# Optimization experiments

Measured on AMD Instinct MI355X. Metric: run time of the kernel, lower is better.

The kernel has to match this reference:

```python
import jax, jax.numpy as jnp
import numpy as np

D_MODEL = 1280
NUM_HEADS = 16
GROUPS = 5
D_K = D_MODEL // NUM_HEADS  # 80
B, S = 4, 1024


def setup_inputs() -> dict:
    key = jax.random.key(0)
    ks = jax.random.split(key, 12)
    lim_dk = 1.0 / np.sqrt(D_K)
    lim_dm = 1.0 / np.sqrt(D_MODEL)
    return {
        "src": jax.random.normal(ks[0], (B, S, D_MODEL), jnp.float32),
        "k": jax.random.normal(ks[1], (B, S, D_MODEL), jnp.float32),
        "v": jax.random.normal(ks[2], (B, S, D_MODEL), jnp.float32),
        # per-head Linear(d_k, d_k) stacked: weight [H, d_k(out), d_k(in)], bias [H, d_k]
        "Wq": jax.random.uniform(ks[3], (NUM_HEADS, D_K, D_K), jnp.float32, -lim_dk, lim_dk),
        "bq": jax.random.uniform(ks[4], (NUM_HEADS, D_K), jnp.float32, -lim_dk, lim_dk),
        "Wk": jax.random.uniform(ks[5], (NUM_HEADS, D_K, D_K), jnp.float32, -lim_dk, lim_dk),
        "bk": jax.random.uniform(ks[6], (NUM_HEADS, D_K), jnp.float32, -lim_dk, lim_dk),
        "Wv": jax.random.uniform(ks[7], (NUM_HEADS, D_K, D_K), jnp.float32, -lim_dk, lim_dk),
        "bv": jax.random.uniform(ks[8], (NUM_HEADS, D_K), jnp.float32, -lim_dk, lim_dk),
        # output Linear(d_model, d_model)
        "Wo": jax.random.uniform(ks[9], (D_MODEL, D_MODEL), jnp.float32, -lim_dm, lim_dm),
        "bo": jax.random.uniform(ks[10], (D_MODEL,), jnp.float32, -lim_dm, lim_dm),
    }


def reference(src, k, v, Wq, bq, Wk, bk, Wv, bv, Wo, bo):
    # NOTE: original module ignores k, v args; q/k/v all derived from src.
    b, s, d = src.shape
    cpg = d // GROUPS
    # channel shuffle: [B,S,G,C] -> [B,S,C,G] -> [B,S,D]
    x = src.reshape(b, s, GROUPS, cpg).swapaxes(-1, -2).reshape(b, s, d)
    # split heads: [B, H, S, d_k]
    xh = x.reshape(b, s, NUM_HEADS, D_K).transpose(0, 2, 1, 3)
    # per-head distinct linears, batched over heads (torch Linear: x @ W.T + b)
    q = jnp.einsum("bhsd,hed->bhse", xh, Wq) + bq[None, :, None, :]
    kk = jnp.einsum("bhsd,hed->bhse", xh, Wk) + bk[None, :, None, :]
    vv = jnp.einsum("bhsd,hed->bhse", xh, Wv) + bv[None, :, None, :]
    scores = jnp.einsum("bhqd,bhkd->bhqk", q, kk) / jnp.sqrt(jnp.float32(D_K))
    p = jax.nn.softmax(scores, axis=-1)
    heads = jnp.einsum("bhqk,bhkd->bhqd", p, vv)
    concat = heads.transpose(0, 2, 1, 3).reshape(b, s, d)
    return concat @ Wo.T + bo
```

## Files before the change

kernel.cpp:

```cpp
#include <hip/hip_runtime.h>
#include <hip/hip_bf16.h>

#define D_MODEL 1280
#define NUM_HEADS 16
#define D_K 80
#define DP 96
#define SEQ 1024
#define BATCH 4
#define BH (BATCH*NUM_HEADS)

typedef __hip_bfloat16 bf16;
typedef short short8 __attribute__((ext_vector_type(8)));
typedef short short4v __attribute__((ext_vector_type(4)));
typedef float f32x4 __attribute__((ext_vector_type(4)));

__device__ __forceinline__ float b2f(bf16 x) { return __bfloat162float(x); }
__device__ __forceinline__ bf16 f2b(float x) { return __float2bfloat16(x); }
__device__ __forceinline__ short bbits(float x) {
    union { bf16 b; short s; } u; u.b = __float2bfloat16(x); return u.s;
}

#define MFMA16(a, b, c) __builtin_amdgcn_mfma_f32_16x16x32_bf16(a, b, c, 0, 0, 0)

__global__ __launch_bounds__(256) void cvtw_kernel(
    const float* __restrict__ Wq, const float* __restrict__ Wk,
    const float* __restrict__ Wv, bf16* __restrict__ Wcat)
{
    int idx = blockIdx.x * 256 + threadIdx.x;
    int col = idx % 96;
    int row = (idx / 96) % 240;
    int h   = idx / (96 * 240);
    int mat = row / 80, e = row % 80;
    const float* W = (mat == 0) ? Wq : (mat == 1) ? Wk : Wv;
    float v = (col < 80) ? W[(size_t)(h * 80 + e) * 80 + col] : 0.f;
    Wcat[idx] = f2b(v);
}

__global__ __launch_bounds__(256) void cvt_kernel(
    const float* __restrict__ Wo, bf16* __restrict__ Wb)
{
    int idx = (blockIdx.x * 256 + threadIdx.x) * 4;
    float4 v = *(const float4*)(Wo + idx);
    Wb[idx]     = f2b(v.x);
    Wb[idx + 1] = f2b(v.y);
    Wb[idx + 2] = f2b(v.z);
    Wb[idx + 3] = f2b(v.w);
}

__global__ __launch_bounds__(256) void qkv_kernel(
    const float* __restrict__ src,
    const float* __restrict__ bq, const float* __restrict__ bk,
    const float* __restrict__ bv, const bf16* __restrict__ Wcat,
    bf16* __restrict__ Qb, bf16* __restrict__ Kb, bf16* __restrict__ Vg)
{
    __shared__ bf16 Xs[128 * 104];
    const int h = blockIdx.y;
    const int b = blockIdx.x >> 3;
    const int s0 = (blockIdx.x & 7) * 128;
    const int tid = threadIdx.x;
    const int wave = tid >> 6, lane = tid & 63;
    const int lquad = lane >> 4, lcol = lane & 15;
    const int bh = b * NUM_HEADS + h;

    #pragma unroll
    for (int it = 0; it < 10; it++) {
        int idx = tid + it * 256;
        int i = idx / 20, rem = idx % 20, c = rem >> 2, q4 = rem & 3;
        float4 v = *(const float4*)(src + (size_t)(b * SEQ + s0 + i) * D_MODEL
                                    + c * 256 + h * 16 + q4 * 4);
        bf16* x = Xs + i * 104 + c;
        x[(q4 * 4 + 0) * 5] = f2b(v.x);
        x[(q4 * 4 + 1) * 5] = f2b(v.y);
        x[(q4 * 4 + 2) * 5] = f2b(v.z);
        x[(q4 * 4 + 3) * 5] = f2b(v.w);
    }
    {
        int i = tid >> 1, half = tid & 1;
        *(uint4*)(Xs + i * 104 + 80 + half * 8) = make_uint4(0, 0, 0, 0);
    }
    __syncthreads();

    short8 xf[2][3];
    #pragma unroll
    for (int mt = 0; mt < 2; mt++)
        #pragma unroll
        for (int ks = 0; ks < 3; ks++)
            xf[mt][ks] = *(const short8*)(Xs + (wave*32 + mt*16 + lcol)*104 + ks*32 + lquad*8);

    const bf16* Wh = Wcat + (size_t)h * 240 * 96;
    const float qscale = 1.4426950408889634f * 0.11180339887498949f;

    #pragma unroll
    for (int mat = 0; mat < 2; mat++) {
        const bf16* Wm = Wh + mat * 80 * 96;
        short8 wf[5][3];
        #pragma unroll
        for (int n = 0; n < 5; n++)
            #pragma unroll
            for (int ks = 0; ks < 3; ks++)
                wf[n][ks] = *(const short8*)(Wm + (n*16 + lcol)*96 + ks*32 + lquad*8);

        f32x4 acc[2][5];
        #pragma unroll
        for (int mt = 0; mt < 2; mt++)
            #pragma unroll
            for (int n = 0; n < 5; n++)
                #pragma unroll
                for (int r = 0; r < 4; r++) acc[mt][n][r] = 0.f;

        #pragma unroll
        for (int ks = 0; ks < 3; ks++)
            #pragma unroll
            for (int n = 0; n < 5; n++) {
                acc[0][n] = MFMA16(xf[0][ks], wf[n][ks], acc[0][n]);
                acc[1][n] = MFMA16(xf[1][ks], wf[n][ks], acc[1][n]);
            }

        const float* bias = (mat == 0) ? bq : bk;
        bf16* Out = (mat == 0) ? Qb : Kb;
        const float scale = (mat == 0) ? qscale : 1.f;
        #pragma unroll
        for (int n = 0; n < 5; n++) {
            float bb = bias[h * 80 + n * 16 + lcol];
            #pragma unroll
            for (int mt = 0; mt < 2; mt++)
                #pragma unroll
                for (int r = 0; r < 4; r++) {
                    int srow = s0 + wave*32 + mt*16 + lquad*4 + r;
                    Out[((size_t)bh * SEQ + srow) * DP + n*16 + lcol] =
                        f2b((acc[mt][n][r] + bb) * scale);
                }
        }
    }
    {
        int i = tid >> 1, half = tid & 1;
        size_t row = ((size_t)bh * SEQ + s0 + i) * DP + 80 + half * 8;
        *(uint4*)(Qb + row) = make_uint4(0, 0, 0, 0);
        *(uint4*)(Kb + row) = make_uint4(0, 0, 0, 0);
    }

    {
        const bf16* Wm = Wh + 2 * 80 * 96;
        short8 wf[5][3];
        #pragma unroll
        for (int m = 0; m < 5; m++)
            #pragma unroll
            for (int ks = 0; ks < 3; ks++)
                wf[m][ks] = *(const short8*)(Wm + (m*16 + lcol)*96 + ks*32 + lquad*8);

        f32x4 acc[5][2];
        #pragma unroll
        for (int m = 0; m < 5; m++)
            #pragma unroll
            for (int nt = 0; nt < 2; nt++)
                #pragma unroll
                for (int r = 0; r < 4; r++) acc[m][nt][r] = 0.f;

        #pragma unroll
        for (int ks = 0; ks < 3; ks++)
            #pragma unroll
            for (int m = 0; m < 5; m++) {
                acc[m][0] = MFMA16(wf[m][ks], xf[0][ks], acc[m][0]);
                acc[m][1] = MFMA16(wf[m][ks], xf[1][ks], acc[m][1]);
            }

        #pragma unroll
        for (int m = 0; m < 5; m++) {
            float4 bb4 = *(const float4*)(bv + h * 80 + m * 16 + lquad * 4);
            float bb[4] = {bb4.x, bb4.y, bb4.z, bb4.w};
            #pragma unroll
            for (int nt = 0; nt < 2; nt++)
                #pragma unroll
                for (int r = 0; r < 4; r++) {
                    int e = m*16 + lquad*4 + r;
                    int token = s0 + wave*32 + nt*16 + lcol;
                    Vg[((size_t)bh * D_K + e) * SEQ + token] =
                        f2b(acc[m][nt][r] + bb[r]);
                }
        }
    }
}

__global__ __launch_bounds__(128) void attn_kernel(
    const bf16* __restrict__ Qb, const bf16* __restrict__ Kb,
    const bf16* __restrict__ Vg, bf16* __restrict__ Cc)
{
    __shared__ char smem[38144];
    bf16* Qs = (bf16*)smem;
    bf16* Ks = (bf16*)(smem + 13312);
    bf16* Vt = (bf16*)(smem + 26624);

    const int tid = threadIdx.x;
    const int wave = tid >> 6, lane = tid & 63;
    const int lquad = lane >> 4, lcol = lane & 15;
    const int bh = blockIdx.x;
    const int b = bh >> 4, h = bh & 15;
    const int q0 = blockIdx.y * 64;

    {
        const uint4* qg = (const uint4*)(Qb + ((size_t)bh * SEQ + q0) * DP);
        #pragma unroll
        for (int i = 0; i < 6; i++) {
            int idx = tid + i * 128, r = idx / 12, c = idx % 12;
            *(uint4*)(Qs + r * 104 + c * 8) = qg[idx];
        }
    }
    __syncthreads();

    short8 qf[2][3];
    #pragma unroll
    for (int nt = 0; nt < 2; nt++)
        #pragma unroll
        for (int ks = 0; ks < 3; ks++)
            qf[nt][ks] = *(const short8*)(Qs + (wave*32 + nt*16 + lcol)*104 + ks*32 + lquad*8);

    f32x4 Oacc[2][5];
    #pragma unroll
    for (int mt = 0; mt < 2; mt++)
        #pragma unroll
        for (int ne = 0; ne < 5; ne++)
            #pragma unroll
            for (int r = 0; r < 4; r++) Oacc[mt][ne][r] = 0.f;

    float lsum[2] = {0.f, 0.f};
    bf16* Pw = (bf16*)(smem + wave * 4608);

    for (int kt = 0; kt < 16; kt++) {
        __syncthreads();
        {
            const uint4* kg = (const uint4*)(Kb + ((size_t)bh * SEQ + kt * 64) * DP);
            #pragma unroll
            for (int i = 0; i < 6; i++) {
                int idx = tid + i * 128, r = idx / 12, c = idx % 12;
                *(uint4*)(Ks + r * 104 + c * 8) = kg[idx];
            }
        }
        #pragma unroll
        for (int i = 0; i < 5; i++) {
            int idx = tid + i * 128;
            int e = idx >> 3, c = idx & 7;
            *(uint4*)(Vt + e * 72 + c * 8) =
                *(const uint4*)(Vg + ((size_t)bh * D_K + e) * SEQ + kt * 64 + c * 8);
        }
        __syncthreads();

        f32x4 st[4][2];
        #pragma unroll
        for (int mt = 0; mt < 4; mt++)
            #pragma unroll
            for (int nt = 0; nt < 2; nt++)
                #pragma unroll
                for (int r = 0; r < 4; r++) st[mt][nt][r] = 0.f;

        #pragma unroll
        for (int ks = 0; ks < 3; ks++) {
            #pragma unroll
            for (int mt = 0; mt < 4; mt++) {
                short8 af = *(const short8*)(Ks + (mt*16 + lcol)*104 + ks*32 + lquad*8);
                st[mt][0] = MFMA16(af, qf[0][ks], st[mt][0]);
                st[mt][1] = MFMA16(af, qf[1][ks], st[mt][1]);
            }
        }

        #pragma unroll
        for (int nt = 0; nt < 2; nt++) {
            #pragma unroll
            for (int mt = 0; mt < 4; mt++) {
                short4v pk;
                #pragma unroll
                for (int r = 0; r < 4; r++) {
                    float p = __builtin_amdgcn_exp2f(st[mt][nt][r]);
                    lsum[nt] += p;
                    pk[r] = bbits(p);
                }
                *(short4v*)(Pw + (nt*16 + lcol)*72 + mt*16 + lquad*4) = pk;
            }
        }

        #pragma unroll
        for (int js = 0; js < 2; js++) {
            short8 pf[2];
            #pragma unroll
            for (int mt = 0; mt < 2; mt++)
                pf[mt] = *(const short8*)(Pw + (mt*16 + lcol)*72 + js*32 + lquad*8);
            #pragma unroll
            for (int ne = 0; ne < 5; ne++) {
                short8 vf = *(const short8*)(Vt + (ne*16 + lcol)*72 + js*32 + lquad*8);
                Oacc[0][ne] = MFMA16(pf[0], vf, Oacc[0][ne]);
                Oacc[1][ne] = MFMA16(pf[1], vf, Oacc[1][ne]);
            }
        }
    }

    float inv[2];
    #pragma unroll
    for (int nt = 0; nt < 2; nt++) {
        float s = lsum[nt];
        s += __shfl_xor(s, 16);
        s += __shfl_xor(s, 32);
        inv[nt] = 1.f / s;
    }
    #pragma unroll
    for (int mt = 0; mt < 2; mt++) {
        f32x4 li;
        #pragma unroll
        for (int r = 0; r < 4; r++)
            li[r] = __shfl(inv[mt], (lane & 48) | (lquad*4 + r));
        #pragma unroll
        for (int ne = 0; ne < 5; ne++)
            #pragma unroll
            for (int r = 0; r < 4; r++) {
                int s_row = q0 + wave*32 + mt*16 + lquad*4 + r;
                int e = ne*16 + lcol;
                Cc[(size_t)(b * SEQ + s_row) * D_MODEL + h * D_K + e] =
                    f2b(Oacc[mt][ne][r] * li[r]);
            }
    }
}

__global__ __launch_bounds__(256) void proj_kernel(
    const bf16* __restrict__ Cc, const bf16* __restrict__ Wb,
    const float* __restrict__ bo, float* __restrict__ out)
{
    __shared__ bf16 As[128 * 72];
    __shared__ bf16 Bs[128 * 72];
    const int tid = threadIdx.x;
    const int wave = tid >> 6, lane = tid & 63;
    const int lquad = lane >> 4, lcol = lane & 15;
    const int t0 = blockIdx.x * 128, o0 = blockIdx.y * 128;
    const int mrow = (wave & 1) * 64, ncol = (wave >> 1) * 64;

    f32x4 acc[4][4];
    #pragma unroll
    for (int mt = 0; mt < 4; mt++)
        #pragma unroll
        for (int nt = 0; nt < 4; nt++)
            #pragma unroll
            for (int r = 0; r < 4; r++) acc[mt][nt][r] = 0.f;

    for (int kc = 0; kc < 20; kc++) {
        __syncthreads();
        #pragma unroll
        for (int i = 0; i < 4; i++) {
            int idx = tid + i * 256;
            int r = idx >> 3, c = idx & 7;
            *(uint4*)(As + r * 72 + c * 8) =
                *(const uint4*)(Cc + (size_t)(t0 + r) * D_MODEL + kc * 64 + c * 8);
            *(uint4*)(Bs + r * 72 + c * 8) =
                *(const uint4*)(Wb + (size_t)(o0 + r) * D_MODEL + kc * 64 + c * 8);
        }
        __syncthreads();
        #pragma unroll
        for (int ks = 0; ks < 2; ks++) {
            short8 am[4], bn[4];
            #pragma unroll
            for (int t = 0; t < 4; t++) {
                am[t] = *(const short8*)(As + (mrow + t*16 + lcol)*72 + ks*32 + lquad*8);
                bn[t] = *(const short8*)(Bs + (ncol + t*16 + lcol)*72 + ks*32 + lquad*8);
            }
            #pragma unroll
            for (int mt = 0; mt < 4; mt++)
                #pragma unroll
                for (int nt = 0; nt < 4; nt++)
                    acc[mt][nt] = MFMA16(am[mt], bn[nt], acc[mt][nt]);
        }
    }

    #pragma unroll
    for (int nt = 0; nt < 4; nt++) {
        float bias = bo[o0 + ncol + nt*16 + lcol];
        #pragma unroll
        for (int mt = 0; mt < 4; mt++)
            #pragma unroll
            for (int r = 0; r < 4; r++)
                out[(size_t)(t0 + mrow + mt*16 + lquad*4 + r) * D_MODEL
                    + o0 + ncol + nt*16 + lcol] = acc[mt][nt][r] + bias;
    }
}

extern "C" void kernel_launch(void* const* d_in, const int* in_sizes, int n_in,
                              void* d_out, int out_size, void* d_ws, size_t ws_size,
                              hipStream_t stream) {
    const float* src = (const float*)d_in[0];
    const float* Wq = (const float*)d_in[3];
    const float* bq = (const float*)d_in[4];
    const float* Wk = (const float*)d_in[5];
    const float* bk = (const float*)d_in[6];
    const float* Wv = (const float*)d_in[7];
    const float* bv = (const float*)d_in[8];
    const float* Wo = (const float*)d_in[9];
    const float* bo = (const float*)d_in[10];
    float* out = (float*)d_out;

    char* ws = (char*)d_ws;
    bf16* Qb = (bf16*)(ws);
    bf16* Kb = (bf16*)(ws + (size_t)12582912);
    bf16* Vg = (bf16*)(ws + (size_t)25165824);
    bf16* Cc = (bf16*)(ws + (size_t)35651584);
    bf16* Wcat = (bf16*)(ws + (size_t)35651584);
    bf16* Wb = (bf16*)(ws + (size_t)46137344);

    cvtw_kernel<<<dim3(1440), 256, 0, stream>>>(Wq, Wk, Wv, Wcat);
    cvt_kernel<<<dim3(D_MODEL * D_MODEL / 1024), 256, 0, stream>>>(Wo, Wb);
    qkv_kernel<<<dim3(BATCH * SEQ / 128, NUM_HEADS), 256, 0, stream>>>(
        src, bq, bk, bv, Wcat, Qb, Kb, Vg);
    attn_kernel<<<dim3(BH, SEQ / 64), 128, 0, stream>>>(Qb, Kb, Vg, Cc);
    proj_kernel<<<dim3(SEQ * BATCH / 128, D_MODEL / 128), 256, 0, stream>>>(
        Cc, Wb, bo, out);
}
```

Before: 198.3 us.

## Load attention K/V/Q fragments directly from global memory, dropping LDS staging

The attention kernel no longer stages Q, K and V tiles in shared memory behind block-wide barriers. Each wave now loads its MFMA operand fragments straight from global memory into registers, keeping only a small per-wave LDS buffer for the probability tile. This removes the LDS round trip and both __syncthreads per key tile and cuts LDS use. In exchange, the two waves in a block each read the same K/V data from global memory or cache, register pressure rises, and loads are no longer coalesced 16-byte transactions across the block.

After: 225.7 us. 13.8% more time.

```diff
diff --git a/kernel.cpp b/kernel.cpp
--- a/kernel.cpp
+++ b/kernel.cpp
@@ -185,34 +185,26 @@
     const bf16* __restrict__ Qb, const bf16* __restrict__ Kb,
     const bf16* __restrict__ Vg, bf16* __restrict__ Cc)
 {
-    __shared__ char smem[38144];
-    bf16* Qs = (bf16*)smem;
-    bf16* Ks = (bf16*)(smem + 13312);
-    bf16* Vt = (bf16*)(smem + 26624);
-
+    __shared__ bf16 Pall[2 * 32 * 72];
     const int tid = threadIdx.x;
     const int wave = tid >> 6, lane = tid & 63;
     const int lquad = lane >> 4, lcol = lane & 15;
     const int bh = blockIdx.x;
     const int b = bh >> 4, h = bh & 15;
     const int q0 = blockIdx.y * 64;
-
-    {
-        const uint4* qg = (const uint4*)(Qb + ((size_t)bh * SEQ + q0) * DP);
-        #pragma unroll
-        for (int i = 0; i < 6; i++) {
-            int idx = tid + i * 128, r = idx / 12, c = idx % 12;
-            *(uint4*)(Qs + r * 104 + c * 8) = qg[idx];
-        }
-    }
-    __syncthreads();
+    bf16* Pw = Pall + wave * 32 * 72;
+
+    const bf16* Kbase = Kb + (size_t)bh * SEQ * DP;
+    const bf16* Vbase = Vg + (size_t)bh * D_K * SEQ;
 
     short8 qf[2][3];
     #pragma unroll
     for (int nt = 0; nt < 2; nt++)
         #pragma unroll
         for (int ks = 0; ks < 3; ks++)
-            qf[nt][ks] = *(const short8*)(Qs + (wave*32 + nt*16 + lcol)*104 + ks*32 + lquad*8);
+            qf[nt][ks] = *(const short8*)(
+                Qb + ((size_t)bh * SEQ + q0 + wave*32 + nt*16 + lcol) * DP
+                   + ks*32 + lquad*8);
 
     f32x4 Oacc[2][5];
     #pragma unroll
@@ -223,26 +215,15 @@
             for (int r = 0; r < 4; r++) Oacc[mt][ne][r] = 0.f;
 
     float lsum[2] = {0.f, 0.f};
-    bf16* Pw = (bf16*)(smem + wave * 4608);
 
     for (int kt = 0; kt < 16; kt++) {
-        __syncthreads();
-        {
-            const uint4* kg = (const uint4*)(Kb + ((size_t)bh * SEQ + kt * 64) * DP);
-            #pragma unroll
-            for (int i = 0; i < 6; i++) {
-                int idx = tid + i * 128, r = idx / 12, c = idx % 12;
-                *(uint4*)(Ks + r * 104 + c * 8) = kg[idx];
-            }
-        }
-        #pragma unroll
-        for (int i = 0; i < 5; i++) {
-            int idx = tid + i * 128;
-            int e = idx >> 3, c = idx & 7;
-            *(uint4*)(Vt + e * 72 + c * 8) =
-                *(const uint4*)(Vg + ((size_t)bh * D_K + e) * SEQ + kt * 64 + c * 8);
-        }
-        __syncthreads();
+        const bf16* Kt = Kbase + (size_t)kt * 64 * DP;
+        short8 af[4][3];
+        #pragma unroll
+        for (int mt = 0; mt < 4; mt++)
+            #pragma unroll
+            for (int ks = 0; ks < 3; ks++)
+                af[mt][ks] = *(const short8*)(Kt + (mt*16 + lcol)*DP + ks*32 + lquad*8);
 
         f32x4 st[4][2];
         #pragma unroll
@@ -253,14 +234,20 @@
                 for (int r = 0; r < 4; r++) st[mt][nt][r] = 0.f;
 
         #pragma unroll
-        for (int ks = 0; ks < 3; ks++) {
+        for (int ks = 0; ks < 3; ks++)
             #pragma unroll
             for (int mt = 0; mt < 4; mt++) {
-                short8 af = *(const short8*)(Ks + (mt*16 + lcol)*104 + ks*32 + lquad*8);
-                st[mt][0] = MFMA16(af, qf[0][ks], st[mt][0]);
-                st[mt][1] = MFMA16(af, qf[1][ks], st[mt][1]);
-            }
-        }
+                st[mt][0] = MFMA16(af[mt][ks], qf[0][ks], st[mt][0]);
+                st[mt][1] = MFMA16(af[mt][ks], qf[1][ks], st[mt][1]);
+            }
+
+        short8 vf[5][2];
+        #pragma unroll
+        for (int ne = 0; ne < 5; ne++)
+            #pragma unroll
+            for (int js = 0; js < 2; js++)
+                vf[ne][js] = *(const short8*)(
+                    Vbase + (size_t)(ne*16 + lcol) * SEQ + kt*64 + js*32 + lquad*8);
 
         #pragma unroll
         for (int nt = 0; nt < 2; nt++) {
@@ -285,9 +272,8 @@
                 pf[mt] = *(const short8*)(Pw + (mt*16 + lcol)*72 + js*32 + lquad*8);
             #pragma unroll
             for (int ne = 0; ne < 5; ne++) {
-                short8 vf = *(const short8*)(Vt + (ne*16 + lcol)*72 + js*32 + lquad*8);
-                Oacc[0][ne] = MFMA16(pf[0], vf, Oacc[0][ne]);
-                Oacc[1][ne] = MFMA16(pf[1], vf, Oacc[1][ne]);
+                Oacc[0][ne] = MFMA16(pf[0], vf[ne][js], Oacc[0][ne]);
+                Oacc[1][ne] = MFMA16(pf[1], vf[ne][js], Oacc[1][ne]);
             }
         }
     }
```
